# Performance work log

Hardware: AMD Instinct MI355X
Metric: run time of the kernel (lower is better)

Reference implementation:

```python
import jax, jax.numpy as jnp
import numpy as np

VOCAB = 50000
N_TOPICS = 200
EMB = 512
BATCH = 2048
TOPK = 20


def setup_inputs() -> dict:
    key = jax.random.key(0)
    k1, k2, k3, k4 = jax.random.split(key, 4)
    alpha = jax.random.normal(k1, (BATCH, N_TOPICS), dtype=jnp.float32)
    doc_bow = jax.random.uniform(k2, (BATCH, VOCAB), dtype=jnp.float32)
    # learned parameters (orthogonal init in the original; scaled normal is fine for a numeric reference)
    topic_embeddings_mat = jax.random.normal(k3, (N_TOPICS, EMB), dtype=jnp.float32) * 0.05
    word_embeddings_mat = jax.random.normal(k4, (EMB, VOCAB), dtype=jnp.float32) * 0.05
    return {
        "alpha": alpha,
        "doc_bow": doc_bow,
        "topic_embeddings_mat": topic_embeddings_mat,
        "word_embeddings_mat": word_embeddings_mat,
    }


def _topk_filter_norm(beta, k):
    # keep top-k entries per topic row, scatter back to [T, V], renormalize to sum 1
    vals, idx = jax.lax.top_k(beta, k)           # [T, k]
    T = beta.shape[0]
    rows = jnp.arange(T)[:, None]
    sparse = jnp.zeros_like(beta).at[rows, idx].set(vals)
    return sparse / vals.sum(-1, keepdims=True)  # [T, V]


def _stdr(beta, k, n_topics):
    # geomloss Sinkhorn(p=2) on single-point clouds == ||x - y||^2 / 2 per pair.
    # Original double loop: sum_{i,j} C(b_i, b_j) / n_topics^2 -> Gram-matrix trick.
    b = _topk_filter_norm(beta, k)               # [T, V]
    sq = jnp.sum(b * b, axis=-1)                 # [T]
    gram = b @ b.T                               # [T, T]
    d2 = jnp.maximum(sq[:, None] + sq[None, :] - 2.0 * gram, 0.0)
    cost = 0.5 * d2
    return cost.sum() / (n_topics * n_topics)


def reference(alpha, doc_bow, topic_embeddings_mat, word_embeddings_mat):
    theta = jax.nn.softmax(alpha, axis=-1)                         # [B, T]
    wt = topic_embeddings_mat @ word_embeddings_mat                # [T, V]
    beta = jax.nn.softmax(wt, axis=1)                              # softmax over vocab
    logits = jnp.log(theta @ beta)                                 # [B, V]
    Re = -jnp.sum(logits * doc_bow, axis=-1)                       # [B]
    STDR = _stdr(beta, TOPK, N_TOPICS)
    return Re, STDR, theta
```

## Files before the change

kernel.cpp:

```cpp
#include <hip/hip_runtime.h>
#include <hip/hip_bf16.h>

#define VOCAB 50000
#define NT    200
#define NTP   256
#define EMB   512
#define BATCH 2048
#define KP    224
#define TK    20

typedef __bf16 bf16x8 __attribute__((ext_vector_type(8)));
typedef float  f32x4  __attribute__((ext_vector_type(4)));

#define OFF_EXPWT   0ull
#define OFF_EXPWTT  40000000ull
#define OFF_THETAB  62400000ull
#define OFF_TOPICA  63317504ull
#define OFF_ROWSUM  63579648ull
#define OFF_STDR    63580448ull
#define OFF_TKV     63580464ull
#define OFF_TKI     63596464ull
#define OFF_TKSQ    63612464ull

__global__ __launch_bounds__(64) void k_theta(const float* __restrict__ alpha,
                                              const float* __restrict__ rowsum,
                                              float* __restrict__ theta_out,
                                              __bf16* __restrict__ theta_b) {
    int b = blockIdx.x;
    int ln = threadIdx.x;
    const float* row = alpha + (size_t)b * NT;
    float a0 = row[ln], a1 = row[ln + 64], a2 = row[ln + 128];
    float a3 = (ln < 8) ? row[ln + 192] : -1e30f;
    float m = fmaxf(fmaxf(a0, a1), fmaxf(a2, a3));
    #pragma unroll
    for (int off = 32; off; off >>= 1) m = fmaxf(m, __shfl_xor(m, off));
    float e0 = __expf(a0 - m), e1 = __expf(a1 - m), e2 = __expf(a2 - m);
    float e3 = (ln < 8) ? __expf(a3 - m) : 0.f;
    float s = e0 + e1 + e2 + e3;
    #pragma unroll
    for (int off = 32; off; off >>= 1) s += __shfl_xor(s, off);
    float inv = 1.f / s;
    float r0 = 1.f / rowsum[ln];
    float r1 = 1.f / rowsum[ln + 64];
    float r2 = 1.f / rowsum[ln + 128];
    float r3 = (ln < 8) ? 1.f / rowsum[ln + 192] : 0.f;
    float* o = theta_out + (size_t)b * NT;
    __bf16* ob = theta_b + (size_t)b * KP;
    o[ln]       = e0 * inv;  ob[ln]       = (__bf16)(e0 * inv * r0);
    o[ln + 64]  = e1 * inv;  ob[ln + 64]  = (__bf16)(e1 * inv * r1);
    o[ln + 128] = e2 * inv;  ob[ln + 128] = (__bf16)(e2 * inv * r2);
    if (ln < 8)       { o[ln + 192] = e3 * inv; ob[ln + 192] = (__bf16)(e3 * inv * r3); }
    else if (ln < 32) { ob[ln + 192] = (__bf16)0.f; }
}

__global__ __launch_bounds__(256) void k_topic_cvt(const float* __restrict__ te,
                                                   __bf16* __restrict__ out) {
    int i = blockIdx.x * 256 + threadIdx.x;
    int t = i >> 9, k = i & 511;
    out[i] = (t < NT) ? (__bf16)te[(size_t)t * EMB + k] : (__bf16)0.f;
}

__global__ __launch_bounds__(256) void k_gemm1(const float* __restrict__ wemb,
                                               const __bf16* __restrict__ Abf,
                                               float* __restrict__ expwt,
                                               __bf16* __restrict__ expwtT,
                                               float* __restrict__ rowsum) {
    __shared__ __align__(16) __bf16 smem[64 * 232];
    __bf16* lB = smem;
    __bf16* tb = smem;
    int tid = threadIdx.x;
    int v0 = blockIdx.x * 64;
    int w = tid >> 6, ln = tid & 63, quad = ln >> 4, c16 = ln & 15;

    f32x4 acc[4][4];
    #pragma unroll
    for (int mi = 0; mi < 4; ++mi)
        #pragma unroll
        for (int ni = 0; ni < 4; ++ni) acc[mi][ni] = (f32x4){0.f, 0.f, 0.f, 0.f};

    for (int ks = 0; ks < EMB / 32; ++ks) {
        int k0 = ks * 32;
        __syncthreads();
        {
            int c = tid & 63, kg = tid >> 6;
            int v = v0 + c;
            bool ok = (v < VOCAB);
            #pragma unroll
            for (int it = 0; it < 8; ++it) {
                int k = kg * 8 + it;
                float val = ok ? wemb[(size_t)(k0 + k) * VOCAB + v] : 0.f;
                lB[c * 40 + k] = (__bf16)val;
            }
        }
        __syncthreads();
        bf16x8 aF[4], bF[4];
        #pragma unroll
        for (int mi = 0; mi < 4; ++mi)
            aF[mi] = *(const bf16x8*)(Abf + (size_t)(w * 64 + mi * 16 + c16) * EMB + k0 + quad * 8);
        #pragma unroll
        for (int ni = 0; ni < 4; ++ni)
            bF[ni] = *(const bf16x8*)(&lB[(ni * 16 + c16) * 40 + quad * 8]);
        #pragma unroll
        for (int mi = 0; mi < 4; ++mi)
            #pragma unroll
            for (int ni = 0; ni < 4; ++ni)
                acc[mi][ni] = __builtin_amdgcn_mfma_f32_16x16x32_bf16(aF[mi], bF[ni], acc[mi][ni], 0, 0, 0);
    }

    __syncthreads();

    #pragma unroll
    for (int mi = 0; mi < 4; ++mi) {
        #pragma unroll
        for (int r = 0; r < 4; ++r) {
            int tt = w * 64 + mi * 16 + quad * 4 + r;
            float rs = 0.f;
            #pragma unroll
            for (int ni = 0; ni < 4; ++ni) {
                int vl = ni * 16 + c16;
                int v = v0 + vl;
                if (v < VOCAB) {
                    if (tt < NT) {
                        float e = __expf(acc[mi][ni][r]);
                        expwt[(size_t)tt * VOCAB + v] = e;
                        rs += e;
                        tb[vl * 232 + tt] = (__bf16)e;
                    } else if (tt < KP) {
                        tb[vl * 232 + tt] = (__bf16)0.f;
                    }
                }
            }
            #pragma unroll
            for (int off = 1; off < 16; off <<= 1) rs += __shfl_xor(rs, off, 16);
            if (tt < NT && c16 == 0) atomicAdd(&rowsum[tt], rs);
        }
    }
    __syncthreads();

    #pragma unroll
    for (int i = 0; i < 7; ++i) {
        int idx = i * 256 + tid;
        int row = idx / 28, seg = idx % 28;
        if (v0 + row < VOCAB)
            *(uint4*)(expwtT + (size_t)(v0 + row) * KP + seg * 8) =
                *(const uint4*)(&tb[row * 232 + seg * 8]);
    }
}

__global__ __launch_bounds__(256) void k_gemm2(const __bf16* __restrict__ thetab,
                                               const __bf16* __restrict__ expwtT,
                                               const float* __restrict__ bow,
                                               float* __restrict__ Re) {
    int tid = threadIdx.x;
    int m0 = blockIdx.x * 128;
    int v0 = blockIdx.y * 128;
    int w = tid >> 6, ln = tid & 63, quad = ln >> 4, c16 = ln & 15;

    const __bf16* aRow[2];
    #pragma unroll
    for (int mi = 0; mi < 2; ++mi)
        aRow[mi] = thetab + (size_t)(m0 + w * 32 + mi * 16 + c16) * KP + quad * 8;
    const __bf16* bRow[8];
    bool vok[8];
    #pragma unroll
    for (int ni = 0; ni < 8; ++ni) {
        int v = v0 + ni * 16 + c16;
        vok[ni] = (v < VOCAB);
        bRow[ni] = expwtT + (size_t)v * KP + quad * 8;
    }

    bf16x8 bz;
    #pragma unroll
    for (int j = 0; j < 8; ++j) bz[j] = (__bf16)0.f;

    f32x4 acc[2][8];
    #pragma unroll
    for (int mi = 0; mi < 2; ++mi)
        #pragma unroll
        for (int ni = 0; ni < 8; ++ni) acc[mi][ni] = (f32x4){0.f, 0.f, 0.f, 0.f};

    bf16x8 aF[2][2], bF[2][8];
#define LOADK(KS, BUF)                                                          \
    {                                                                           \
        _Pragma("unroll") for (int mi = 0; mi < 2; ++mi)                        \
            aF[BUF][mi] = *(const bf16x8*)(aRow[mi] + (KS) * 32);               \
        _Pragma("unroll") for (int ni = 0; ni < 8; ++ni)                        \
            bF[BUF][ni] = vok[ni] ? *(const bf16x8*)(bRow[ni] + (KS) * 32) : bz;\
    }

    LOADK(0, 0);
    #pragma unroll
    for (int ks = 0; ks < KP / 32; ++ks) {
        int cur = ks & 1;
        if (ks < KP / 32 - 1) LOADK(ks + 1, (ks + 1) & 1);
        #pragma unroll
        for (int mi = 0; mi < 2; ++mi)
            #pragma unroll
            for (int ni = 0; ni < 8; ++ni)
                acc[mi][ni] = __builtin_amdgcn_mfma_f32_16x16x32_bf16(aF[cur][mi], bF[cur][ni],
                                                                      acc[mi][ni], 0, 0, 0);
    }
#undef LOADK

    #pragma unroll
    for (int mi = 0; mi < 2; ++mi) {
        #pragma unroll
        for (int r = 0; r < 4; ++r) {
            int b = m0 + w * 32 + mi * 16 + quad * 4 + r;
            float s = 0.f;
            #pragma unroll
            for (int ni = 0; ni < 8; ++ni) {
                int v = v0 + ni * 16 + c16;
                if (v < VOCAB)
                    s += __logf(acc[mi][ni][r]) * bow[(size_t)b * VOCAB + v];
            }
            #pragma unroll
            for (int off = 1; off < 16; off <<= 1) s += __shfl_xor(s, off, 16);
            if (c16 == 0) atomicAdd(&Re[b], -s);
        }
    }
}

__global__ __launch_bounds__(256) void k_topk(const float* __restrict__ expwt,
                                              float* __restrict__ tkv,
                                              int* __restrict__ tki,
                                              float* __restrict__ tksq) {
    __shared__ float lv[256 * TK];
    __shared__ int   li[256 * TK];
    __shared__ int   head[256];
    __shared__ float redv[256];
    __shared__ int   redi[256];
    __shared__ float selv[TK];
    __shared__ int   seli[TK];
    int t = blockIdx.x, tid = threadIdx.x;
    const float* row = expwt + (size_t)t * VOCAB;

    float tv[TK]; int ti[TK];
    #pragma unroll
    for (int i = 0; i < TK; ++i) { tv[i] = -1e30f; ti[i] = 0; }

    for (int v = tid; v < VOCAB; v += 256) {
        float val = row[v];
        if (val > tv[TK - 1]) {
            #pragma unroll
            for (int i = TK - 1; i >= 1; --i) {
                bool sh  = val > tv[i - 1];
                bool put = val > tv[i];
                float nv = sh ? tv[i - 1] : (put ? val : tv[i]);
                int  nix = sh ? ti[i - 1] : (put ? v   : ti[i]);
                tv[i] = nv; ti[i] = nix;
            }
            if (val > tv[0]) { tv[0] = val; ti[0] = v; }
        }
    }
    #pragma unroll
    for (int i = 0; i < TK; ++i) { lv[tid * TK + i] = tv[i]; li[tid * TK + i] = ti[i]; }
    head[tid] = 0;
    __syncthreads();

    for (int sel = 0; sel < TK; ++sel) {
        int h = head[tid];
        redv[tid] = (h < TK) ? lv[tid * TK + h] : -1e30f;
        redi[tid] = tid;
        __syncthreads();
        for (int s2 = 128; s2 > 0; s2 >>= 1) {
            if (tid < s2) {
                if (redv[tid + s2] > redv[tid]) {
                    redv[tid] = redv[tid + s2]; redi[tid] = redi[tid + s2];
                }
            }
            __syncthreads();
        }
        if (tid == 0) {
            int wt = redi[0];
            int hh = head[wt];
            selv[sel] = lv[wt * TK + hh];
            seli[sel] = li[wt * TK + hh];
            head[wt] = hh + 1;
        }
        __syncthreads();
    }

    if (tid == 0) {
        float sum = 0.f;
        #pragma unroll
        for (int i = 0; i < TK; ++i) sum += selv[i];
        float inv = 1.f / sum, sq = 0.f;
        #pragma unroll
        for (int i = 0; i < TK; ++i) {
            float nv = selv[i] * inv;
            tkv[t * TK + i] = nv;
            tki[t * TK + i] = seli[i];
            sq += nv * nv;
        }
        tksq[t] = sq;
    }
}

__global__ __launch_bounds__(256) void k_pairs(const float* __restrict__ tkv,
                                               const int* __restrict__ tki,
                                               const float* __restrict__ tksq,
                                               float* __restrict__ stdr) {
    int p = blockIdx.x * 256 + threadIdx.x;
    float contrib = 0.f;
    if (p < NT * NT) {
        int i = p / NT, j = p % NT;
        float vi[TK], vj[TK]; int ii[TK], ij[TK];
        #pragma unroll
        for (int a = 0; a < TK; ++a) { vi[a] = tkv[i * TK + a]; ii[a] = tki[i * TK + a]; }
        #pragma unroll
        for (int a = 0; a < TK; ++a) { vj[a] = tkv[j * TK + a]; ij[a] = tki[j * TK + a]; }
        float g = 0.f;
        for (int a = 0; a < TK; ++a) {
            #pragma unroll
            for (int b = 0; b < TK; ++b)
                if (ii[a] == ij[b]) g += vi[a] * vj[b];
        }
        float d2 = fmaxf(tksq[i] + tksq[j] - 2.f * g, 0.f);
        contrib = 0.5f * d2;
    }
    __shared__ float red[256];
    red[threadIdx.x] = contrib;
    __syncthreads();
    for (int s = 128; s; s >>= 1) {
        if (threadIdx.x < s) red[threadIdx.x] += red[threadIdx.x + s];
        __syncthreads();
    }
    if (threadIdx.x == 0) atomicAdd(stdr, red[0]);
}

__global__ void k_final(const float* __restrict__ stdr, float* __restrict__ out) {
    out[0] = stdr[0] * (1.f / (float)(NT * NT));
}

extern "C" void kernel_launch(void* const* d_in, const int* in_sizes, int n_in,
                              void* d_out, int out_size, void* d_ws, size_t ws_size,
                              hipStream_t stream) {
    const float* alpha = (const float*)d_in[0];
    const float* bow   = (const float*)d_in[1];
    const float* temb  = (const float*)d_in[2];
    const float* wemb  = (const float*)d_in[3];
    float* out = (float*)d_out;
    char* ws = (char*)d_ws;

    float*  expwt  = (float*)(ws + OFF_EXPWT);
    __bf16* expwtT = (__bf16*)(ws + OFF_EXPWTT);
    __bf16* thetab = (__bf16*)(ws + OFF_THETAB);
    __bf16* topA   = (__bf16*)(ws + OFF_TOPICA);
    float*  rowsum = (float*)(ws + OFF_ROWSUM);
    float*  stdr   = (float*)(ws + OFF_STDR);
    float*  tkv    = (float*)(ws + OFF_TKV);
    int*    tki    = (int*)(ws + OFF_TKI);
    float*  tksq   = (float*)(ws + OFF_TKSQ);

    float* Re        = out;
    float* stdr_out  = out + BATCH;
    float* theta_out = out + BATCH + 1;

    hipMemsetAsync(Re, 0, BATCH * sizeof(float), stream);
    hipMemsetAsync(ws + OFF_ROWSUM, 0, 804, stream);

    k_topic_cvt<<<512, 256, 0, stream>>>(temb, topA);
    k_gemm1<<<(VOCAB + 63) / 64, 256, 0, stream>>>(wemb, topA, expwt, expwtT, rowsum);
    k_theta<<<BATCH, 64, 0, stream>>>(alpha, rowsum, theta_out, thetab);
    k_gemm2<<<dim3(BATCH / 128, (VOCAB + 127) / 128), 256, 0, stream>>>(thetab, expwtT, bow, Re);
    k_topk<<<NT, 256, 0, stream>>>(expwt, tkv, tki, tksq);
    k_pairs<<<(NT * NT + 255) / 256, 256, 0, stream>>>(tkv, tki, tksq, stdr);
    k_final<<<1, 1, 0, stream>>>(stdr, stdr_out);
}
```

Baseline: 1.390 ms.

## Stage gemm2 tiles through LDS with direct global-to-LDS loads and swizzle

Replaces per-lane direct global fragment loads in the theta×expwtT GEMM with double-buffered LDS staging using global_load_lds, an XOR swizzle to avoid bank conflicts, and a remapped block order for better L2 locality. Occupancy hint of 3 blocks per CU is added. This aims to cut redundant uncoalesced global traffic for B rows shared across waves, at the cost of LDS usage and a barrier per k-step. The epilogue reading bow and computing log is unchanged and may still dominate.

```diff
diff --git a/kernel.cpp b/kernel.cpp
--- a/kernel.cpp
+++ b/kernel.cpp
@@ -21,6 +21,14 @@
 #define OFF_TKV     63580464ull
 #define OFF_TKI     63596464ull
 #define OFF_TKSQ    63612464ull
+
+__device__ __forceinline__ void gll16(const void* g, void* l) {
+    __builtin_amdgcn_global_load_lds(
+        (const __attribute__((address_space(1))) unsigned int*)g,
+        (__attribute__((address_space(3))) unsigned int*)l, 16, 0, 0);
+}
+
+#define FRAG(arr, r, q) (*(const bf16x8*)(&(arr)[(((r) * 4 + ((q) ^ (((r) >> 1) & 3))) * 8)]))
 
 __global__ __launch_bounds__(64) void k_theta(const float* __restrict__ alpha,
                                               const float* __restrict__ rowsum,
@@ -147,66 +155,70 @@
     }
 }
 
-__global__ __launch_bounds__(256) void k_gemm2(const __bf16* __restrict__ thetab,
-                                               const __bf16* __restrict__ expwtT,
-                                               const float* __restrict__ bow,
-                                               float* __restrict__ Re) {
+__global__ __launch_bounds__(256, 3) void k_gemm2(const __bf16* __restrict__ thetab,
+                                                  const __bf16* __restrict__ expwtT,
+                                                  const float* __restrict__ bow,
+                                                  float* __restrict__ Re) {
+    __shared__ __align__(16) __bf16 sA[2][128 * 32];
+    __shared__ __align__(16) __bf16 sB[2][128 * 32];
     int tid = threadIdx.x;
-    int m0 = blockIdx.x * 128;
-    int v0 = blockIdx.y * 128;
-    int w = tid >> 6, ln = tid & 63, quad = ln >> 4, c16 = ln & 15;
-
-    const __bf16* aRow[2];
+
+    int flat = blockIdx.x + blockIdx.y * 16;
+    int swz  = (flat & 7) * 782 + (flat >> 3);
+    int m0 = (swz & 15) * 128;
+    int v0 = (swz >> 4) * 128;
+
+    int wv = tid >> 6, ln = tid & 63, quad = ln >> 4, c16 = ln & 15;
+
+    f32x4 acc[2][8];
     #pragma unroll
     for (int mi = 0; mi < 2; ++mi)
-        aRow[mi] = thetab + (size_t)(m0 + w * 32 + mi * 16 + c16) * KP + quad * 8;
-    const __bf16* bRow[8];
-    bool vok[8];
-    #pragma unroll
-    for (int ni = 0; ni < 8; ++ni) {
-        int v = v0 + ni * 16 + c16;
-        vok[ni] = (v < VOCAB);
-        bRow[ni] = expwtT + (size_t)v * KP + quad * 8;
-    }
-
-    bf16x8 bz;
-    #pragma unroll
-    for (int j = 0; j < 8; ++j) bz[j] = (__bf16)0.f;
-
-    f32x4 acc[2][8];
-    #pragma unroll
-    for (int mi = 0; mi < 2; ++mi)
         #pragma unroll
         for (int ni = 0; ni < 8; ++ni) acc[mi][ni] = (f32x4){0.f, 0.f, 0.f, 0.f};
 
-    bf16x8 aF[2][2], bF[2][8];
-#define LOADK(KS, BUF)                                                          \
+#define STAGE2(buf, ks)                                                         \
     {                                                                           \
-        _Pragma("unroll") for (int mi = 0; mi < 2; ++mi)                        \
-            aF[BUF][mi] = *(const bf16x8*)(aRow[mi] + (KS) * 32);               \
-        _Pragma("unroll") for (int ni = 0; ni < 8; ++ni)                        \
-            bF[BUF][ni] = vok[ni] ? *(const bf16x8*)(bRow[ni] + (KS) * 32) : bz;\
-    }
-
-    LOADK(0, 0);
-    #pragma unroll
+        int k0_ = (ks) * 32;                                                    \
+        _Pragma("unroll") for (int j = 0; j < 2; ++j) {                         \
+            int s   = j * 256 + wv * 64 + ln;                                   \
+            int row = s >> 2;                                                   \
+            int ul  = (s & 3) ^ ((s >> 3) & 3);                                 \
+            gll16(thetab + (size_t)(m0 + row) * KP + k0_ + ul * 8,              \
+                  &sA[buf][(j * 256 + wv * 64) * 8]);                           \
+            int vr = v0 + row; vr = (vr < VOCAB) ? vr : (VOCAB - 1);            \
+            gll16(expwtT + (size_t)vr * KP + k0_ + ul * 8,                      \
+                  &sB[buf][(j * 256 + wv * 64) * 8]);                           \
+        }                                                                       \
+    }
+
+    STAGE2(0, 0);
+    __syncthreads();
+
     for (int ks = 0; ks < KP / 32; ++ks) {
         int cur = ks & 1;
-        if (ks < KP / 32 - 1) LOADK(ks + 1, (ks + 1) & 1);
+        if (ks < KP / 32 - 1) STAGE2(cur ^ 1, ks + 1);
+        bf16x8 aF[2], bF[8];
         #pragma unroll
         for (int mi = 0; mi < 2; ++mi)
+            aF[mi] = FRAG(sA[cur], wv * 32 + mi * 16 + c16, quad);
+        #pragma unroll
+        for (int ni = 0; ni < 8; ++ni)
+            bF[ni] = FRAG(sB[cur], ni * 16 + c16, quad);
+        #pragma unroll
+        for (int mi = 0; mi < 2; ++mi)
             #pragma unroll
             for (int ni = 0; ni < 8; ++ni)
-                acc[mi][ni] = __builtin_amdgcn_mfma_f32_16x16x32_bf16(aF[cur][mi], bF[cur][ni],
+                acc[mi][ni] = __builtin_amdgcn_mfma_f32_16x16x32_bf16(aF[mi], bF[ni],
                                                                       acc[mi][ni], 0, 0, 0);
-    }
-#undef LOADK
+        __syncthreads();
+    }
+#undef STAGE2
 
     #pragma unroll
     for (int mi = 0; mi < 2; ++mi) {
         #pragma unroll
         for (int r = 0; r < 4; ++r) {
-            int b = m0 + w * 32 + mi * 16 + quad * 4 + r;
+            int b = m0 + wv * 32 + mi * 16 + quad * 4 + r;
             float s = 0.f;
             #pragma unroll
             for (int ni = 0; ni < 8; ++ni) {
```

Measured after the change: 1.221 ms. 1.14x faster.
